# Performance work log

Hardware: AMD Instinct MI355X
Metric: run time of the kernel (lower is better)

The kernel has to match this reference:

```python
import jax, jax.numpy as jnp
import numpy as np


def setup_inputs() -> dict:
    key = jax.random.key(0)
    B, T_TEXT, MAX_LEN = 32, 512, 4096
    # per-token durations in frames, uniform in [1, 8) -> repeats in {1..8}
    durations = jax.random.uniform(key, (B, T_TEXT), dtype=jnp.float32, minval=1.0, maxval=8.0)
    return {"durations": durations, "max_len": MAX_LEN}


def reference(durations, max_len):
    # Faithful translation of Variance_Block.Length_Regulate:
    #   repeats = (durations.float() + 0.5).long()          (truncation == round for positive d)
    #   reps_cumsum = cumsum(pad(repeats, left=1))
    #   align[b, t, j] = (cumsum[:, j] <= t) & (cumsum[:, j+1] > t)
    repeats = (durations + 0.5).astype(jnp.int32)            # [B, T_text]
    ends = jnp.cumsum(repeats, axis=1)                       # reps_cumsum[:, 1:]
    starts = ends - repeats                                  # reps_cumsum[:, :-1]
    range_ = jnp.arange(max_len, dtype=jnp.int32)            # [max_len]
    # [B, max_len, T_text] boolean alignment via broadcast compare
    alignments = (starts[:, None, :] <= range_[None, :, None]) & (ends[:, None, :] > range_[None, :, None])
    return alignments.astype(jnp.float32)
```

## Files before the change

kernel.cpp:

```cpp
#include <hip/hip_runtime.h>


#define T_TEXT 512
#define ROWS 8
#define WBLOCK 256

__global__ void lr_scan_kernel(const float* __restrict__ dur,
                               int* __restrict__ ends) {
    __shared__ int s[T_TEXT];
    const int b = blockIdx.x;
    const int tid = threadIdx.x;
    float d = dur[b * T_TEXT + tid];
    s[tid] = (int)(d + 0.5f);
    __syncthreads();
    for (int off = 1; off < T_TEXT; off <<= 1) {
        int v = s[tid];
        int add = (tid >= off) ? s[tid - off] : 0;
        __syncthreads();
        s[tid] = v + add;
        __syncthreads();
    }
    ends[b * T_TEXT + tid] = s[tid];
}

__global__ __launch_bounds__(WBLOCK) void lr_write_kernel(
        const int* __restrict__ ends_all,
        float* __restrict__ out,
        int max_len) {
    __shared__ int s_ends[T_TEXT];
    __shared__ int s_j[ROWS];

    const int b  = blockIdx.y;
    const int t0 = blockIdx.x * ROWS;
    const int tid = threadIdx.x;

    const int* ends = ends_all + b * T_TEXT;
    s_ends[tid]       = ends[tid];
    s_ends[tid + 256] = ends[tid + 256];
    __syncthreads();

    if (tid < ROWS) {
        int t = t0 + tid;
        int j = -1;
        if (t < s_ends[T_TEXT - 1]) {
            int lo = 0, hi = T_TEXT;
            while (lo < hi) {
                int mid = (lo + hi) >> 1;
                if (s_ends[mid] > t) hi = mid; else lo = mid + 1;
            }
            j = lo;
        }
        s_j[tid] = j;
    }
    __syncthreads();

    float4* outv = (float4*)(out + ((size_t)b * max_len + t0) * T_TEXT);
    const int nvec = ROWS * (T_TEXT / 4);
    for (int f = tid; f < nvec; f += WBLOCK) {
        int r = f >> 7;
        int c = (f & 127) << 2;
        int j = s_j[r];
        float4 v = make_float4(0.f, 0.f, 0.f, 0.f);
        int k = j - c;
        if ((unsigned)k < 4u) ((float*)&v)[k] = 1.0f;
        if (t0 + r < max_len) outv[f] = v;
    }
}

extern "C" void kernel_launch(void* const* d_in, const int* in_sizes, int n_in,
                              void* d_out, int out_size, void* d_ws, size_t ws_size,
                              hipStream_t stream) {
    const float* dur = (const float*)d_in[0];
    float* out = (float*)d_out;

    const int BT = in_sizes[0];
    const int B = BT / T_TEXT;
    const int max_len = out_size / BT;

    int* ends = (int*)d_ws;

    lr_scan_kernel<<<B, T_TEXT, 0, stream>>>(dur, ends);

    dim3 grid((max_len + ROWS - 1) / ROWS, B);
    lr_write_kernel<<<grid, WBLOCK, 0, stream>>>(ends, out, max_len);
}
```

Measured before the change: 269.2 us.

## Replace dense write kernel with memset plus scatter of ones

Drops the separate binary-search write kernel. The output is now zeroed with hipMemsetAsync, and the scan kernel scatters the 1.0 values straight into each token's column for its frame range. This removes the workspace round-trip and the per-row search, and leaves the bulk zero fill to the runtime memset. In exchange the scatter writes are strided, hitting one float per row, and only 32 blocks run, so the ones are written with little parallelism.

```diff
diff --git a/kernel.cpp b/kernel.cpp
--- a/kernel.cpp
+++ b/kernel.cpp
@@ -2,17 +2,19 @@
 
 
 #define T_TEXT 512
-#define ROWS 8
-#define WBLOCK 256
 
-__global__ void lr_scan_kernel(const float* __restrict__ dur,
-                               int* __restrict__ ends) {
+__global__ __launch_bounds__(T_TEXT) void lr_scan_scatter(
+        const float* __restrict__ dur,
+        float* __restrict__ out,
+        int max_len) {
     __shared__ int s[T_TEXT];
     const int b = blockIdx.x;
     const int tid = threadIdx.x;
-    float d = dur[b * T_TEXT + tid];
-    s[tid] = (int)(d + 0.5f);
+
+    const int rep = (int)(dur[b * T_TEXT + tid] + 0.5f);
+    s[tid] = rep;
     __syncthreads();
+
     for (int off = 1; off < T_TEXT; off <<= 1) {
         int v = s[tid];
         int add = (tid >= off) ? s[tid - off] : 0;
@@ -20,50 +22,14 @@
         s[tid] = v + add;
         __syncthreads();
     }
-    ends[b * T_TEXT + tid] = s[tid];
-}
 
-__global__ __launch_bounds__(WBLOCK) void lr_write_kernel(
-        const int* __restrict__ ends_all,
-        float* __restrict__ out,
-        int max_len) {
-    __shared__ int s_ends[T_TEXT];
-    __shared__ int s_j[ROWS];
+    int end = s[tid];
+    int start = end - rep;
+    if (end > max_len) end = max_len;
 
-    const int b  = blockIdx.y;
-    const int t0 = blockIdx.x * ROWS;
-    const int tid = threadIdx.x;
-
-    const int* ends = ends_all + b * T_TEXT;
-    s_ends[tid]       = ends[tid];
-    s_ends[tid + 256] = ends[tid + 256];
-    __syncthreads();
-
-    if (tid < ROWS) {
-        int t = t0 + tid;
-        int j = -1;
-        if (t < s_ends[T_TEXT - 1]) {
-            int lo = 0, hi = T_TEXT;
-            while (lo < hi) {
-                int mid = (lo + hi) >> 1;
-                if (s_ends[mid] > t) hi = mid; else lo = mid + 1;
-            }
-            j = lo;
-        }
-        s_j[tid] = j;
-    }
-    __syncthreads();
-
-    float4* outv = (float4*)(out + ((size_t)b * max_len + t0) * T_TEXT);
-    const int nvec = ROWS * (T_TEXT / 4);
-    for (int f = tid; f < nvec; f += WBLOCK) {
-        int r = f >> 7;
-        int c = (f & 127) << 2;
-        int j = s_j[r];
-        float4 v = make_float4(0.f, 0.f, 0.f, 0.f);
-        int k = j - c;
-        if ((unsigned)k < 4u) ((float*)&v)[k] = 1.0f;
-        if (t0 + r < max_len) outv[f] = v;
+    float* col = out + ((size_t)b * max_len) * T_TEXT + tid;
+    for (int t = start; t < end; ++t) {
+        col[(size_t)t * T_TEXT] = 1.0f;
     }
 }
 
@@ -77,10 +43,7 @@
     const int B = BT / T_TEXT;
     const int max_len = out_size / BT;
 
-    int* ends = (int*)d_ws;
+    hipMemsetAsync(d_out, 0, (size_t)out_size * sizeof(float), stream);
 
-    lr_scan_kernel<<<B, T_TEXT, 0, stream>>>(dur, ends);
-
-    dim3 grid((max_len + ROWS - 1) / ROWS, B);
-    lr_write_kernel<<<grid, WBLOCK, 0, stream>>>(ends, out, max_len);
+    lr_scan_scatter<<<B, T_TEXT, 0, stream>>>(dur, out, max_len);
 }
```

New measurement: 253.9 us. 5.7% less time.
